# Kernel optimization log

Hardware: AMD Instinct MI355X
Metric: run time of the kernel (lower is better)

Reference implementation:

```python
import jax, jax.numpy as jnp
import numpy as np

B, N, D, H = 4, 2048, 1024, 16
DH = D // H


def setup_inputs() -> dict:
    key = jax.random.key(0)
    ks = jax.random.split(key, 9)
    std = 0.02
    return {
        "x": jax.random.normal(ks[0], (B, N, D), dtype=jnp.float32),
        "Wq": jax.random.normal(ks[1], (D, D), dtype=jnp.float32) * std,
        "bq": jnp.zeros((D,), dtype=jnp.float32),
        "Wk": jax.random.normal(ks[2], (D, D), dtype=jnp.float32) * std,
        "bk": jnp.zeros((D,), dtype=jnp.float32),
        "Wv": jax.random.normal(ks[3], (D, D), dtype=jnp.float32) * std,
        "bv": jnp.zeros((D,), dtype=jnp.float32),
        "Wo": jax.random.normal(ks[4], (D, D), dtype=jnp.float32) * std,
        "bo": jnp.zeros((D,), dtype=jnp.float32),
        "k": 8,
        "dilation": 2,
    }


def _dilated_mask(n_q, n_k, k, dilation):
    # allowed[i, j] = True iff |j - i| <= k*dilation and (j - i) % dilation == 0
    i = jnp.arange(n_q)[:, None]
    j = jnp.arange(n_k)[None, :]
    d = j - i
    return (jnp.abs(d) <= k * dilation) & ((d % dilation) == 0)


def reference(x, Wq, bq, Wk, bk, Wv, bv, Wo, bo, k, dilation):
    b, n_q, d_model = x.shape
    n_heads = H
    d_head = d_model // n_heads
    # self-attention: context = x
    q = (x @ Wq + bq).reshape(b, n_q, n_heads, d_head).transpose(0, 2, 1, 3)  # (B,H,Nq,Dh)
    kk = (x @ Wk + bk).reshape(b, n_q, n_heads, d_head).transpose(0, 2, 1, 3)
    v = (x @ Wv + bv).reshape(b, n_q, n_heads, d_head).transpose(0, 2, 1, 3)

    scale = 1.0 / np.sqrt(d_head).astype(np.float32)
    scores = jnp.einsum("bhqd,bhkd->bhqk", q, kk) * scale  # (B,H,Nq,Nk)
    allowed = _dilated_mask(n_q, n_q, k, dilation)  # (Nq,Nk)
    scores = jnp.where(allowed[None, None], scores, -jnp.inf)
    attn = jax.nn.softmax(scores, axis=-1)
    out = jnp.einsum("bhqk,bhkd->bhqd", attn, v)  # (B,H,Nq,Dh)
    out = out.transpose(0, 2, 1, 3).reshape(b, n_q, d_model)
    return out @ Wo + bo
```

## Files before the change

kernel.cpp:

```cpp
#include <hip/hip_runtime.h>
#include <hip/hip_bf16.h>
#include <hip/hip_fp16.h>
#include <stdint.h>

using bf16 = __hip_bfloat16;

typedef __bf16    bf16x8 __attribute__((ext_vector_type(8)));
typedef float     floatx4 __attribute__((ext_vector_type(4)));
typedef _Float16  f16x8 __attribute__((ext_vector_type(8)));

typedef __attribute__((address_space(3))) void as3_void;
typedef __attribute__((address_space(1))) void as1_void;

#define GLD_LDS16(gp, lp) \
  __builtin_amdgcn_global_load_lds((as1_void*)(uintptr_t)(gp), (as3_void*)(uintptr_t)(lp), 16, 0, 0)

#define FENCE() asm volatile("" ::: "memory")
#define BAR()   do { FENCE(); __builtin_amdgcn_s_barrier(); FENCE(); } while (0)
#define WAITL0() do { asm volatile("s_waitcnt lgkmcnt(0)" ::: "memory"); \
                      __builtin_amdgcn_sched_barrier(0); } while (0)

__global__ __launch_bounds__(256) void prep_kernel(
    const float* __restrict__ x,
    const float* __restrict__ Wq, const float* __restrict__ Wk,
    const float* __restrict__ Wv, const float* __restrict__ Wo,
    bf16* __restrict__ xbf, bf16* __restrict__ WTqkv, bf16* __restrict__ WoT) {
  __shared__ float tile[64 * 68];
  const int blk = blockIdx.x;
  const int tid = threadIdx.x;
  if (blk < 1024) {
    const int z = blk >> 8, t = blk & 255;
    const float* src = (z == 0) ? Wq : (z == 1) ? Wk : (z == 2) ? Wv : Wo;
    bf16* dst = (z < 3) ? (WTqkv + (size_t)z * 1024 * 1024) : WoT;
    const int nbase = (t & 15) * 64, kbase = (t >> 4) * 64;
    const int r1 = tid >> 4, c1 = tid & 15;
#pragma unroll
    for (int it = 0; it < 4; ++it) {
      const int row = r1 + it * 16;
      const float4 v = *(const float4*)(src + (size_t)(kbase + row) * 1024 + nbase + c1 * 4);
      *(float4*)(tile + row * 68 + c1 * 4) = v;
    }
    __syncthreads();
    const int c2 = tid & 7, n2 = tid >> 3;
#pragma unroll
    for (int it2 = 0; it2 < 2; ++it2) {
      const int n = n2 + it2 * 32;
      bf16 o[8];
#pragma unroll
      for (int s = 0; s < 8; ++s) o[s] = (bf16)tile[(8 * c2 + s) * 68 + n];
      *(uint4*)(dst + (size_t)(nbase + n) * 1024 + kbase + 8 * c2) = *(const uint4*)o;
    }
  } else {
    const size_t basei = ((size_t)(blk - 1024) * 256 + tid) * 16;
#pragma unroll
    for (int h = 0; h < 2; ++h) {
      const float4 a = *(const float4*)(x + basei + h * 8);
      const float4 b = *(const float4*)(x + basei + h * 8 + 4);
      bf16 o[8] = {(bf16)a.x, (bf16)a.y, (bf16)a.z, (bf16)a.w,
                   (bf16)b.x, (bf16)b.y, (bf16)b.z, (bf16)b.w};
      *(uint4*)(xbf + basei + h * 8) = *(const uint4*)o;
    }
  }
}

#define SAU(bufi, u, kt) \
  GLD_LDS16(A + abase + (uint64_t)(u) * 65536 + (uint64_t)(kt) * 64, \
            (char*)(&As[bufi][0]) + (u) * 8192 + ldst)
#define SBU(bufi, u, kt) \
  GLD_LDS16(Bt + bbase + (uint64_t)(u) * 65536 + (uint64_t)(kt) * 64, \
            (char*)(&Bs[bufi][0]) + (u) * 8192 + ldst)

#define RDA2(bufi, mb) do { \
    const char* _p = (const char*)(&As[bufi][0]) + (wm * 128 + (mb) * 16 + l16) * 128; \
    af[0][0] = *(const bf16x8*)(_p + pcb0); \
    af[0][1] = *(const bf16x8*)(_p + pcb1); \
    af[1][0] = *(const bf16x8*)(_p + 2048 + pcb0); \
    af[1][1] = *(const bf16x8*)(_p + 2048 + pcb1); \
  } while (0)

#define RDB3(bufi) do { \
    const char* _p = (const char*)(&Bs[bufi][0]) + (wn * 48 + l16) * 128; \
    bfr[0][0] = *(const bf16x8*)(_p + pcb0); \
    bfr[0][1] = *(const bf16x8*)(_p + pcb1); \
    bfr[1][0] = *(const bf16x8*)(_p + 2048 + pcb0); \
    bfr[1][1] = *(const bf16x8*)(_p + 2048 + pcb1); \
    bfr[2][0] = *(const bf16x8*)(_p + 4096 + pcb0); \
    bfr[2][1] = *(const bf16x8*)(_p + 4096 + pcb1); \
  } while (0)

#define MMQ12(mb) do { \
    _Pragma("unroll") for (int _i = 0; _i < 2; ++_i) \
      _Pragma("unroll") for (int _j = 0; _j < 3; ++_j) \
        _Pragma("unroll") for (int _k = 0; _k < 2; ++_k) \
          acc[(mb) + _i][_j] = __builtin_amdgcn_mfma_f32_16x16x32_bf16( \
              af[_i][_k], bfr[_j][_k], acc[(mb) + _i][_j], 0, 0, 0); \
  } while (0)

__global__ __launch_bounds__(512, 2) void gemm_qkv_8ph(
    const bf16* __restrict__ A, const bf16* __restrict__ Bt,
    const float* __restrict__ b0, const float* __restrict__ b1, const float* __restrict__ b2,
    __half* __restrict__ qkv) {
  const int t    = threadIdx.x;
  const int m0   = blockIdx.x * 256;
  const int n0   = blockIdx.y * 192;
  const int lane = t & 63;
  const int wave = t >> 6;
  const int wm   = wave >> 2;
  const int wn   = wave & 3;
  const int quad = lane >> 4;
  const int l16  = lane & 15;

  __shared__ alignas(16) bf16 As[2][256 * 64];
  __shared__ alignas(16) bf16 Bs[2][192 * 64];

  const int srt = t >> 3;
  const int sct = ((t & 7) ^ (srt & 7)) << 3;
  const uint64_t abase = (uint64_t)(m0 + srt) * 1024 + sct;
  const uint64_t bbase = (uint64_t)(n0 + srt) * 1024 + sct;
  const int ldst = t * 16;

  const int pcb0 = ((quad) ^ (l16 & 7)) << 4;
  const int pcb1 = ((4 + quad) ^ (l16 & 7)) << 4;

  floatx4 acc[8][3];
#pragma unroll
  for (int i = 0; i < 8; ++i)
#pragma unroll
    for (int j = 0; j < 3; ++j) {
      floatx4 z = {0.f, 0.f, 0.f, 0.f};
      acc[i][j] = z;
    }
  bf16x8 af[2][2], bfr[3][2];

  SBU(0, 0, 0); SBU(0, 1, 0); SBU(0, 2, 0);
  SAU(0, 0, 0); SAU(0, 1, 0); SAU(0, 2, 0); SAU(0, 3, 0);
  SBU(1, 0, 1); SBU(1, 1, 1); SBU(1, 2, 1);
  SAU(1, 0, 1); SAU(1, 2, 1);
  asm volatile("s_waitcnt vmcnt(5)" ::: "memory");
  BAR();

  for (int i = 0; i < 8; ++i) {
    const int kt1 = 2 * i + 1;
    const int kt2 = 2 * i + 2;
    const int kt3 = 2 * i + 3;
    const bool pf = (i < 7);

    RDA2(0, 0); RDB3(0);
    SAU(1, 1, kt1); SAU(1, 3, kt1);
    BAR(); WAITL0();
    __builtin_amdgcn_s_setprio(1); MMQ12(0); __builtin_amdgcn_s_setprio(0);
    BAR();

    RDA2(0, 2);
    if (pf) { SBU(0, 0, kt2); SBU(0, 1, kt2); }
    BAR(); WAITL0();
    __builtin_amdgcn_s_setprio(1); MMQ12(2); __builtin_amdgcn_s_setprio(0);
    BAR();

    RDA2(0, 4);
    if (pf) { SBU(0, 2, kt2); SAU(0, 0, kt2); SAU(0, 2, kt2); }
    BAR(); WAITL0();
    __builtin_amdgcn_s_setprio(1); MMQ12(4); __builtin_amdgcn_s_setprio(0);
    BAR();

    RDA2(0, 6);
    BAR(); WAITL0();
    __builtin_amdgcn_s_setprio(1); MMQ12(6); __builtin_amdgcn_s_setprio(0);
    if (pf) { asm volatile("s_waitcnt vmcnt(5)" ::: "memory"); }
    else    { asm volatile("s_waitcnt vmcnt(0)" ::: "memory"); }
    BAR();

    RDA2(1, 0); RDB3(1);
    if (pf) { SAU(0, 1, kt2); SAU(0, 3, kt2); }
    BAR(); WAITL0();
    __builtin_amdgcn_s_setprio(1); MMQ12(0); __builtin_amdgcn_s_setprio(0);
    BAR();

    RDA2(1, 2);
    if (pf) { SBU(1, 0, kt3); SBU(1, 1, kt3); }
    BAR(); WAITL0();
    __builtin_amdgcn_s_setprio(1); MMQ12(2); __builtin_amdgcn_s_setprio(0);
    BAR();

    RDA2(1, 4);
    if (pf) { SBU(1, 2, kt3); SAU(1, 0, kt3); SAU(1, 2, kt3); }
    BAR(); WAITL0();
    __builtin_amdgcn_s_setprio(1); MMQ12(4); __builtin_amdgcn_s_setprio(0);
    BAR();

    RDA2(1, 6);
    BAR(); WAITL0();
    __builtin_amdgcn_s_setprio(1); MMQ12(6); __builtin_amdgcn_s_setprio(0);
    if (pf) { asm volatile("s_waitcnt vmcnt(5)" ::: "memory"); }
    BAR();
  }

  float bvs[3];
#pragma unroll
  for (int nj = 0; nj < 3; ++nj) {
    const int n = n0 + wn * 48 + nj * 16 + l16;
    const int which = n >> 10;
    const int c = n & 1023;
    bvs[nj] = ((which == 0) ? b0 : (which == 1) ? b1 : b2)[c];
  }
  _Float16* stg = (_Float16*)(&As[0][0]);
#pragma unroll
  for (int mi = 0; mi < 8; ++mi) {
#pragma unroll
    for (int nj = 0; nj < 3; ++nj)
#pragma unroll
      for (int r = 0; r < 4; ++r)
        stg[(wm * 16 + quad * 4 + r) * 200 + wn * 48 + nj * 16 + l16] =
            (_Float16)(acc[mi][nj][r] + bvs[nj]);
    BAR();
#pragma unroll
    for (int rep = 0; rep < 2; ++rep) {
      const int cc = t + rep * 512;
      if (cc < 768) {
        const int rl = cc / 24;
        const int ch = cc - rl * 24;
        const int mrow = m0 + (rl >> 4) * 128 + mi * 16 + (rl & 15);
        const f16x8 v = *(const f16x8*)(stg + rl * 200 + ch * 8);
        *(f16x8*)((_Float16*)qkv + (size_t)mrow * 3072 + n0 + ch * 8) = v;
      }
    }
    BAR();
  }
}

__global__ __launch_bounds__(256) void gemm_proj(
    const bf16* __restrict__ A, const bf16* __restrict__ Bt,
    const float* __restrict__ bias, float* __restrict__ fout) {
  const int tid  = threadIdx.x;
  const int m0   = blockIdx.x * 128;
  const int n0   = blockIdx.y * 128;
  const int lane = tid & 63;
  const int wave = tid >> 6;
  const int wr   = (wave >> 1) * 64;
  const int wc   = (wave & 1) * 64;
  const int quad = lane >> 4;
  const int l16  = lane & 15;

  __shared__ alignas(16) bf16 As[128 * 64];
  __shared__ alignas(16) bf16 Bs[128 * 64];

  const int srow = tid >> 3;
  const int cg   = (tid & 7) ^ (srow & 7);
  const uint64_t aoff = (uint64_t)(m0 + srow) * 1024 + cg * 8;
  const uint64_t boff = (uint64_t)(n0 + srow) * 1024 + cg * 8;

  floatx4 acc[4][4];
#pragma unroll
  for (int i = 0; i < 4; ++i)
#pragma unroll
    for (int j = 0; j < 4; ++j) {
      floatx4 z = {0.f, 0.f, 0.f, 0.f};
      acc[i][j] = z;
    }

  for (int k0 = 0; k0 < 1024; k0 += 64) {
    __syncthreads();
#pragma unroll
    for (int it = 0; it < 4; ++it) {
      GLD_LDS16(A + aoff + (uint64_t)it * 32768 + k0, (char*)As + it * 4096 + tid * 16);
      GLD_LDS16(Bt + boff + (uint64_t)it * 32768 + k0, (char*)Bs + it * 4096 + tid * 16);
    }
    __syncthreads();

#pragma unroll
    for (int kc = 0; kc < 2; ++kc) {
      bf16x8 af[4], bfr[4];
#pragma unroll
      for (int i = 0; i < 4; ++i) {
        const int mrow = wr + i * 16 + l16;
        const int pca  = (kc * 4 + quad) ^ (mrow & 7);
        af[i] = *(const bf16x8*)(As + mrow * 64 + pca * 8);
        const int nrow = wc + i * 16 + l16;
        const int pcb  = (kc * 4 + quad) ^ (nrow & 7);
        bfr[i] = *(const bf16x8*)(Bs + nrow * 64 + pcb * 8);
      }
#pragma unroll
      for (int i = 0; i < 4; ++i)
#pragma unroll
        for (int j = 0; j < 4; ++j)
          acc[i][j] = __builtin_amdgcn_mfma_f32_16x16x32_bf16(af[i], bfr[j], acc[i][j], 0, 0, 0);
    }
  }

#pragma unroll
  for (int i = 0; i < 4; ++i)
#pragma unroll
    for (int j = 0; j < 4; ++j)
#pragma unroll
      for (int r = 0; r < 4; ++r) {
        const int m = m0 + wr + i * 16 + quad * 4 + r;
        const int n = n0 + wc + j * 16 + l16;
        fout[(uint64_t)m * 1024 + n] = acc[i][j][r] + bias[n];
      }
}

#define RMAXA 32
#define VTS 176
#define PS  104

__global__ __launch_bounds__(256) void dilated_attn_mfma_kernel(
    const __half* __restrict__ qkv, bf16* __restrict__ attn_out,
    const int* __restrict__ kptr, const int* __restrict__ dptr) {
  const int tid  = threadIdx.x;
  const int wave = tid >> 6, lane = tid & 63;
  const int quad = lane >> 4, l16 = lane & 15;
  const int bh = blockIdx.x >> 5;
  const int Q0 = (blockIdx.x & 31) * 64;
  const int b  = bh >> 4, h = bh & 15;
  const int kk  = kptr[0];
  const int dil = dptr[0];
  const int R   = kk * dil;
  const size_t xb = (size_t)b * 2048;
  const int qo = h * 64, ko = 1024 + h * 64, vo = 2048 + h * 64;
  const _Float16* Xh = (const _Float16*)qkv;

  __shared__ alignas(16) _Float16 smem[64 * VTS + 4 * 16 * PS];
  _Float16* VT = smem;
  _Float16* Pw = smem + 64 * VTS + wave * 16 * PS;

  const bool fast = (R <= RMAXA) && (dil >= 1);

  if (fast) {
    {
      const int nch = (64 * VTS + 4 * 16 * PS) / 8;
      const f16x8 z = {0, 0, 0, 0, 0, 0, 0, 0};
      for (int c = tid; c < nch; c += 256) ((f16x8*)smem)[c] = z;
    }
    __syncthreads();

    const int jlo = Q0 - R;
    const int lo = (jlo > 0) ? jlo : 0;
    const int hi = (Q0 + 63 + R < 2047) ? Q0 + 63 + R : 2047;
    const int nrows = hi - lo + 1;
    for (int idx = tid; idx < nrows * 8; idx += 256) {
      const int r = idx >> 3, c = idx & 7;
      const int j = lo + r;
      const f16x8 v = *(const f16x8*)(Xh + (xb + j) * 3072 + vo + c * 8);
      const int col = j - jlo + 32;
#pragma unroll
      for (int s = 0; s < 8; ++s) VT[(c * 8 + s) * VTS + col] = v[s];
    }
    __syncthreads();

    const int i0 = Q0 + wave * 16;
    const f16x8 a0 = *(const f16x8*)(Xh + (xb + i0 + l16) * 3072 + qo + quad * 8);
    const f16x8 a1 = *(const f16x8*)(Xh + (xb + i0 + l16) * 3072 + qo + 32 + quad * 8);

    const int nkt = (16 + 2 * R + 15) >> 4;
    const int jw0 = i0 - R;
    float lsum[4] = {0.f, 0.f, 0.f, 0.f};
    const floatx4 zf = {0.f, 0.f, 0.f, 0.f};

    for (int kt = 0; kt < nkt; ++kt) {
      const int j0 = jw0 + 16 * kt;
      const int jn = j0 + l16;
      const int jc = (jn < 0) ? 0 : (jn > 2047 ? 2047 : jn);
      const f16x8 k0v = *(const f16x8*)(Xh + (xb + jc) * 3072 + ko + quad * 8);
      const f16x8 k1v = *(const f16x8*)(Xh + (xb + jc) * 3072 + ko + 32 + quad * 8);
      floatx4 s4 = __builtin_amdgcn_mfma_f32_16x16x32_f16(a0, k0v, zf, 0, 0, 0);
      s4 = __builtin_amdgcn_mfma_f32_16x16x32_f16(a1, k1v, s4, 0, 0, 0);
#pragma unroll
      for (int r = 0; r < 4; ++r) {
        const int m = quad * 4 + r;
        const int d = jn - (i0 + m);
        const bool valid = ((unsigned)jn < 2048u) && (d >= -R) && (d <= R) && (d % dil == 0);
        const float pe = valid ? __expf(s4[r] * 0.125f) : 0.f;
        lsum[r] += pe;
        Pw[m * PS + kt * 16 + l16] = (_Float16)pe;
      }
    }
#pragma unroll
    for (int r = 0; r < 4; ++r) {
      lsum[r] += __shfl_xor(lsum[r], 1);
      lsum[r] += __shfl_xor(lsum[r], 2);
      lsum[r] += __shfl_xor(lsum[r], 4);
      lsum[r] += __shfl_xor(lsum[r], 8);
    }

    const int nkc = (nkt * 16 + 31) >> 5;
    floatx4 o[4] = {zf, zf, zf, zf};
    const int vbase = 16 * wave + 32;
    for (int c = 0; c < nkc; ++c) {
      const f16x8 pa = *(const f16x8*)(Pw + l16 * PS + c * 32 + quad * 8);
#pragma unroll
      for (int t = 0; t < 4; ++t) {
        const f16x8 vb = *(const f16x8*)(VT + (t * 16 + l16) * VTS + vbase + c * 32 + quad * 8);
        o[t] = __builtin_amdgcn_mfma_f32_16x16x32_f16(pa, vb, o[t], 0, 0, 0);
      }
    }

#pragma unroll
    for (int t = 0; t < 4; ++t) {
#pragma unroll
      for (int r = 0; r < 4; ++r)
        Pw[(quad * 4 + r) * PS + t * 16 + l16] = (_Float16)(o[t][r] / lsum[r]);
    }
    const int orow = lane >> 2, oseg = lane & 3;
#pragma unroll
    for (int hseg = 0; hseg < 2; ++hseg) {
      const f16x8 ov = *(const f16x8*)(Pw + orow * PS + oseg * 16 + hseg * 8);
      bf16 ob[8];
#pragma unroll
      for (int s = 0; s < 8; ++s) ob[s] = (bf16)(float)ov[s];
      *(uint4*)(attn_out + (xb + i0 + orow) * 1024 + h * 64 + oseg * 16 + hseg * 8) =
          *(const uint4*)ob;
    }
    return;
  }

  if (tid < 64) {
    const int i = Q0 + tid;
    float l = 0.f;
    float oacc[64];
#pragma unroll
    for (int u = 0; u < 64; ++u) oacc[u] = 0.f;
    float qv[64];
#pragma unroll
    for (int u = 0; u < 64; ++u) qv[u] = (float)Xh[(xb + i) * 3072 + qo + u];
    for (int tt = -kk; tt <= kk; ++tt) {
      const int j = i + (int)((long long)tt * dil);
      if (j < 0 || j >= 2048) continue;
      float s = 0.f;
      for (int u = 0; u < 64; ++u) s += qv[u] * (float)Xh[(xb + j) * 3072 + ko + u];
      const float pe = __expf(s * 0.125f);
      l += pe;
      for (int u = 0; u < 64; ++u) oacc[u] += pe * (float)Xh[(xb + j) * 3072 + vo + u];
    }
    for (int u = 0; u < 64; ++u)
      attn_out[(xb + i) * 1024 + h * 64 + u] = (bf16)(oacc[u] / l);
  }
}

extern "C" void kernel_launch(void* const* d_in, const int* in_sizes, int n_in,
                              void* d_out, int out_size, void* d_ws, size_t ws_size,
                              hipStream_t stream) {
  const float* x  = (const float*)d_in[0];
  const float* Wq = (const float*)d_in[1];
  const float* bq = (const float*)d_in[2];
  const float* Wk = (const float*)d_in[3];
  const float* bk = (const float*)d_in[4];
  const float* Wv = (const float*)d_in[5];
  const float* bv = (const float*)d_in[6];
  const float* Wo = (const float*)d_in[7];
  const float* bo = (const float*)d_in[8];
  const int* kp   = (const int*)d_in[9];
  const int* dp   = (const int*)d_in[10];
  float* out = (float*)d_out;

  bf16*   xbf   = (bf16*)d_ws;
  bf16*   WTqkv = xbf + 8388608;
  bf16*   WoT   = WTqkv + 3072 * 1024;
  __half* qkv   = (__half*)(WoT + 1024 * 1024);
  bf16*   attnO = xbf;

  prep_kernel<<<dim3(3072), 256, 0, stream>>>(x, Wq, Wk, Wv, Wo, xbf, WTqkv, WoT);

  gemm_qkv_8ph<<<dim3(32, 16), 512, 0, stream>>>(xbf, WTqkv, bq, bk, bv, qkv);

  dilated_attn_mfma_kernel<<<dim3(2048), 256, 0, stream>>>(qkv, attnO, kp, dp);

  gemm_proj<<<dim3(64, 8), 256, 0, stream>>>(attnO, WoT, bo, out);
}
```

Baseline: 208.2 us.

## Reshape QKV GEMM wave tiling to 4x2 and merge pipeline phases

The wave grid of the QKV GEMM changes from 2x4 to 4x2, so each wave computes a 64x96 sub-tile instead of 128x48. This lowers LDS fragment reads per MFMA and allows each half-iteration to use 2 larger MMA phases instead of 4, which cuts the number of barriers. The load prefetch schedule and vmcnt thresholds are rebalanced to match. The epilogue stages the whole 256x192 tile in LDS at once and writes it out in one pass, replacing the per-row-block loop with its repeated barriers. The cost is more live B-fragment registers and less interleaving between prefetch and compute.

```diff
diff --git a/kernel.cpp b/kernel.cpp
--- a/kernel.cpp
+++ b/kernel.cpp
@@ -65,32 +65,30 @@
 
 #define SAU(bufi, u, kt) \
   GLD_LDS16(A + abase + (uint64_t)(u) * 65536 + (uint64_t)(kt) * 64, \
-            (char*)(&As[bufi][0]) + (u) * 8192 + ldst)
+            (char*)Asp[bufi] + (u) * 8192 + ldst)
 #define SBU(bufi, u, kt) \
   GLD_LDS16(Bt + bbase + (uint64_t)(u) * 65536 + (uint64_t)(kt) * 64, \
-            (char*)(&Bs[bufi][0]) + (u) * 8192 + ldst)
+            (char*)Bsp[bufi] + (u) * 8192 + ldst)
 
 #define RDA2(bufi, mb) do { \
-    const char* _p = (const char*)(&As[bufi][0]) + (wm * 128 + (mb) * 16 + l16) * 128; \
+    const char* _p = (const char*)Asp[bufi] + (wm * 64 + (mb) * 16 + l16) * 128; \
     af[0][0] = *(const bf16x8*)(_p + pcb0); \
     af[0][1] = *(const bf16x8*)(_p + pcb1); \
     af[1][0] = *(const bf16x8*)(_p + 2048 + pcb0); \
     af[1][1] = *(const bf16x8*)(_p + 2048 + pcb1); \
   } while (0)
 
-#define RDB3(bufi) do { \
-    const char* _p = (const char*)(&Bs[bufi][0]) + (wn * 48 + l16) * 128; \
-    bfr[0][0] = *(const bf16x8*)(_p + pcb0); \
-    bfr[0][1] = *(const bf16x8*)(_p + pcb1); \
-    bfr[1][0] = *(const bf16x8*)(_p + 2048 + pcb0); \
-    bfr[1][1] = *(const bf16x8*)(_p + 2048 + pcb1); \
-    bfr[2][0] = *(const bf16x8*)(_p + 4096 + pcb0); \
-    bfr[2][1] = *(const bf16x8*)(_p + 4096 + pcb1); \
+#define RDB6(bufi) do { \
+    const char* _p = (const char*)Bsp[bufi] + (wn * 96 + l16) * 128; \
+    _Pragma("unroll") for (int _j = 0; _j < 6; ++_j) { \
+      bfr[_j][0] = *(const bf16x8*)(_p + _j * 2048 + pcb0); \
+      bfr[_j][1] = *(const bf16x8*)(_p + _j * 2048 + pcb1); \
+    } \
   } while (0)
 
-#define MMQ12(mb) do { \
+#define MMQ24(mb) do { \
     _Pragma("unroll") for (int _i = 0; _i < 2; ++_i) \
-      _Pragma("unroll") for (int _j = 0; _j < 3; ++_j) \
+      _Pragma("unroll") for (int _j = 0; _j < 6; ++_j) \
         _Pragma("unroll") for (int _k = 0; _k < 2; ++_k) \
           acc[(mb) + _i][_j] = __builtin_amdgcn_mfma_f32_16x16x32_bf16( \
               af[_i][_k], bfr[_j][_k], acc[(mb) + _i][_j], 0, 0, 0); \
@@ -105,13 +103,14 @@
   const int n0   = blockIdx.y * 192;
   const int lane = t & 63;
   const int wave = t >> 6;
-  const int wm   = wave >> 2;
-  const int wn   = wave & 3;
+  const int wm   = wave >> 1;
+  const int wn   = wave & 1;
   const int quad = lane >> 4;
   const int l16  = lane & 15;
 
-  __shared__ alignas(16) bf16 As[2][256 * 64];
-  __shared__ alignas(16) bf16 Bs[2][192 * 64];
+  __shared__ alignas(16) char smem[114688];
+  bf16* const Asp[2] = {(bf16*)smem, (bf16*)(smem + 32768)};
+  bf16* const Bsp[2] = {(bf16*)(smem + 65536), (bf16*)(smem + 90112)};
 
   const int srt = t >> 3;
   const int sct = ((t & 7) ^ (srt & 7)) << 3;
@@ -122,21 +121,20 @@
   const int pcb0 = ((quad) ^ (l16 & 7)) << 4;
   const int pcb1 = ((4 + quad) ^ (l16 & 7)) << 4;
 
-  floatx4 acc[8][3];
-#pragma unroll
-  for (int i = 0; i < 8; ++i)
-#pragma unroll
-    for (int j = 0; j < 3; ++j) {
+  floatx4 acc[4][6];
+#pragma unroll
+  for (int i = 0; i < 4; ++i)
+#pragma unroll
+    for (int j = 0; j < 6; ++j) {
       floatx4 z = {0.f, 0.f, 0.f, 0.f};
       acc[i][j] = z;
     }
-  bf16x8 af[2][2], bfr[3][2];
+  bf16x8 af[2][2], bfr[6][2];
 
   SBU(0, 0, 0); SBU(0, 1, 0); SBU(0, 2, 0);
   SAU(0, 0, 0); SAU(0, 1, 0); SAU(0, 2, 0); SAU(0, 3, 0);
   SBU(1, 0, 1); SBU(1, 1, 1); SBU(1, 2, 1);
-  SAU(1, 0, 1); SAU(1, 2, 1);
-  asm volatile("s_waitcnt vmcnt(5)" ::: "memory");
+  asm volatile("s_waitcnt vmcnt(3)" ::: "memory");
   BAR();
 
   for (int i = 0; i < 8; ++i) {
@@ -145,86 +143,59 @@
     const int kt3 = 2 * i + 3;
     const bool pf = (i < 7);
 
-    RDA2(0, 0); RDB3(0);
-    SAU(1, 1, kt1); SAU(1, 3, kt1);
+    RDA2(0, 0); RDB6(0);
+    SAU(1, 0, kt1); SAU(1, 1, kt1); SAU(1, 2, kt1); SAU(1, 3, kt1);
     BAR(); WAITL0();
-    __builtin_amdgcn_s_setprio(1); MMQ12(0); __builtin_amdgcn_s_setprio(0);
+    __builtin_amdgcn_s_setprio(1); MMQ24(0); __builtin_amdgcn_s_setprio(0);
     BAR();
 
     RDA2(0, 2);
-    if (pf) { SBU(0, 0, kt2); SBU(0, 1, kt2); }
+    if (pf) { SBU(0, 0, kt2); SBU(0, 1, kt2); SBU(0, 2, kt2); }
     BAR(); WAITL0();
-    __builtin_amdgcn_s_setprio(1); MMQ12(2); __builtin_amdgcn_s_setprio(0);
-    BAR();
-
-    RDA2(0, 4);
-    if (pf) { SBU(0, 2, kt2); SAU(0, 0, kt2); SAU(0, 2, kt2); }
-    BAR(); WAITL0();
-    __builtin_amdgcn_s_setprio(1); MMQ12(4); __builtin_amdgcn_s_setprio(0);
-    BAR();
-
-    RDA2(0, 6);
-    BAR(); WAITL0();
-    __builtin_amdgcn_s_setprio(1); MMQ12(6); __builtin_amdgcn_s_setprio(0);
-    if (pf) { asm volatile("s_waitcnt vmcnt(5)" ::: "memory"); }
+    __builtin_amdgcn_s_setprio(1); MMQ24(2); __builtin_amdgcn_s_setprio(0);
+    if (pf) { asm volatile("s_waitcnt vmcnt(3)" ::: "memory"); }
     else    { asm volatile("s_waitcnt vmcnt(0)" ::: "memory"); }
     BAR();
 
-    RDA2(1, 0); RDB3(1);
-    if (pf) { SAU(0, 1, kt2); SAU(0, 3, kt2); }
+    RDA2(1, 0); RDB6(1);
+    if (pf) { SAU(0, 0, kt2); SAU(0, 1, kt2); SAU(0, 2, kt2); SAU(0, 3, kt2); }
     BAR(); WAITL0();
-    __builtin_amdgcn_s_setprio(1); MMQ12(0); __builtin_amdgcn_s_setprio(0);
+    __builtin_amdgcn_s_setprio(1); MMQ24(0); __builtin_amdgcn_s_setprio(0);
     BAR();
 
     RDA2(1, 2);
-    if (pf) { SBU(1, 0, kt3); SBU(1, 1, kt3); }
+    if (pf) { SBU(1, 0, kt3); SBU(1, 1, kt3); SBU(1, 2, kt3); }
     BAR(); WAITL0();
-    __builtin_amdgcn_s_setprio(1); MMQ12(2); __builtin_amdgcn_s_setprio(0);
+    __builtin_amdgcn_s_setprio(1); MMQ24(2); __builtin_amdgcn_s_setprio(0);
+    if (pf) { asm volatile("s_waitcnt vmcnt(3)" ::: "memory"); }
     BAR();
-
-    RDA2(1, 4);
-    if (pf) { SBU(1, 2, kt3); SAU(1, 0, kt3); SAU(1, 2, kt3); }
-    BAR(); WAITL0();
-    __builtin_amdgcn_s_setprio(1); MMQ12(4); __builtin_amdgcn_s_setprio(0);
-    BAR();
-
-    RDA2(1, 6);
-    BAR(); WAITL0();
-    __builtin_amdgcn_s_setprio(1); MMQ12(6); __builtin_amdgcn_s_setprio(0);
-    if (pf) { asm volatile("s_waitcnt vmcnt(5)" ::: "memory"); }
-    BAR();
-  }
-
-  float bvs[3];
-#pragma unroll
-  for (int nj = 0; nj < 3; ++nj) {
-    const int n = n0 + wn * 48 + nj * 16 + l16;
+  }
+
+  float bvs[6];
+#pragma unroll
+  for (int nj = 0; nj < 6; ++nj) {
+    const int n = n0 + wn * 96 + nj * 16 + l16;
     const int which = n >> 10;
     const int c = n & 1023;
     bvs[nj] = ((which == 0) ? b0 : (which == 1) ? b1 : b2)[c];
   }
-  _Float16* stg = (_Float16*)(&As[0][0]);
-#pragma unroll
-  for (int mi = 0; mi < 8; ++mi) {
-#pragma unroll
-    for (int nj = 0; nj < 3; ++nj)
+  _Float16* stg = (_Float16*)smem;
+#pragma unroll
+  for (int mb = 0; mb < 4; ++mb)
+#pragma unroll
+    for (int nj = 0; nj < 6; ++nj)
 #pragma unroll
       for (int r = 0; r < 4; ++r)
-        stg[(wm * 16 + quad * 4 + r) * 200 + wn * 48 + nj * 16 + l16] =
-            (_Float16)(acc[mi][nj][r] + bvs[nj]);
-    BAR();
-#pragma unroll
-    for (int rep = 0; rep < 2; ++rep) {
-      const int cc = t + rep * 512;
-      if (cc < 768) {
-        const int rl = cc / 24;
-        const int ch = cc - rl * 24;
-        const int mrow = m0 + (rl >> 4) * 128 + mi * 16 + (rl & 15);
-        const f16x8 v = *(const f16x8*)(stg + rl * 200 + ch * 8);
-        *(f16x8*)((_Float16*)qkv + (size_t)mrow * 3072 + n0 + ch * 8) = v;
-      }
-    }
-    BAR();
+        stg[(wm * 64 + mb * 16 + quad * 4 + r) * 200 + wn * 96 + nj * 16 + l16] =
+            (_Float16)(acc[mb][nj][r] + bvs[nj]);
+  BAR();
+#pragma unroll
+  for (int rep = 0; rep < 12; ++rep) {
+    const int cc = t + rep * 512;
+    const int rl = cc / 24;
+    const int ch = cc - rl * 24;
+    const f16x8 v = *(const f16x8*)(stg + rl * 200 + ch * 8);
+    *(f16x8*)((_Float16*)qkv + (size_t)(m0 + rl) * 3072 + n0 + ch * 8) = v;
   }
 }
 
```

Result: no change. 206.4 us (-0.9%).
